# Kernel optimization log

Measured on AMD Instinct MI355X. Metric: run time of the kernel, lower is better.

## Reference

```python
import jax, jax.numpy as jnp
import numpy as np

# Dims
B_, L_, IN_ = 16, 8192, 57
DM, DS, HD, EXP, NL, OUT = 64, 32, 32, 2, 2, 6
DI = EXP * DM            # 128 inner dim
NH = DI // HD            # 4 heads
DPROJ = 2 * DI + 2 * DS + NH  # z, x, B, C, dt


def setup_inputs() -> dict:
    key = jax.random.key(0)
    ks = jax.random.split(key, 8)
    def rn(k, shape, scale=0.02):
        return jax.random.normal(k, shape, dtype=jnp.float32) * scale
    return {
        "x": jax.random.normal(ks[0], (B_, L_, IN_), dtype=jnp.float32),
        "W_in": rn(ks[1], (IN_, DM)),
        "b_in": jnp.zeros((DM,), jnp.float32),
        "in_proj_W": rn(ks[2], (NL, DM, DPROJ)),
        "in_proj_b": jnp.zeros((NL, DPROJ), jnp.float32),
        "A_log": jnp.log(jnp.broadcast_to(jnp.arange(1, NH + 1, dtype=jnp.float32), (NL, NH))),
        "D": jnp.ones((NL, NH), jnp.float32),
        "dt_bias": rn(ks[3], (NL, NH), 0.1),
        "out_proj_W": rn(ks[4], (NL, DI, DM)),
        "out_proj_b": jnp.zeros((NL, DM), jnp.float32),
        "cls_W": rn(ks[5], (DM, OUT)),
        "cls_b": jnp.zeros((OUT,), jnp.float32),
    }


def _mamba_layer(x, W, b, A_log, D, dt_bias, Wo, bo):
    """SISO Mamba3-style selective scan block. x: [B, L, DM]."""
    Bsz, L, _ = x.shape
    zxbcdt = x @ W + b                               # [B, L, DPROJ]
    z, xin, Bm, Cm, dt = jnp.split(
        zxbcdt, [DI, 2 * DI, 2 * DI + DS, 2 * DI + 2 * DS], axis=-1)
    dt = jax.nn.softplus(dt + dt_bias)               # [B, L, NH]
    A = -jnp.exp(A_log)                              # [NH], per-head scalar (SISO)
    xin = jax.nn.silu(xin).reshape(Bsz, L, NH, HD)   # [B, L, NH, HD]
    Bm = jax.nn.silu(Bm)                             # [B, L, DS]
    Cm = jax.nn.silu(Cm)                             # [B, L, DS]
    decay = jnp.exp(dt * A)                          # [B, L, NH]

    def step(h, inp):
        # h: [B, NH, HD, DS]
        xt, bt, ct, dtt, dect = inp
        h = dect[:, :, None, None] * h + (dtt[:, :, None] * xt)[..., None] * bt[:, None, None, :]
        yt = jnp.einsum('bhpn,bn->bhp', h, ct)       # [B, NH, HD]
        return h, yt

    h0 = jnp.zeros((Bsz, NH, HD, DS), x.dtype)
    xs = (jnp.moveaxis(xin, 1, 0), jnp.moveaxis(Bm, 1, 0), jnp.moveaxis(Cm, 1, 0),
          jnp.moveaxis(dt, 1, 0), jnp.moveaxis(decay, 1, 0))
    _, ys = jax.lax.scan(step, h0, xs)               # [L, B, NH, HD]
    y = jnp.moveaxis(ys, 0, 1) + D[None, None, :, None] * xin
    y = y.reshape(Bsz, L, DI) * jax.nn.silu(z)       # gated output
    return y @ Wo + bo                               # [B, L, DM]


def reference(x, W_in, b_in, in_proj_W, in_proj_b, A_log, D, dt_bias,
              out_proj_W, out_proj_b, cls_W, cls_b):
    h = x @ W_in + b_in                              # linear_in
    for l in range(NL):                              # residual Mamba stack
        h = h + _mamba_layer(h, in_proj_W[l], in_proj_b[l], A_log[l], D[l],
                             dt_bias[l], out_proj_W[l], out_proj_b[l])
    pooled = h.mean(axis=1)                          # AdaptiveAvgPool1d(1)
    return pooled @ cls_W + cls_b                    # classifier [B, OUT]
```

## Files before the change

kernel.cpp:

```cpp
#include <hip/hip_runtime.h>

#define BSZ   16
#define LSEQ  8192
#define DMDL  64
#define DSD   32
#define HDD   32
#define NHD   4
#define DIN   128
#define NLAY  2
#define NOUTC 6
#define DPRJ  324
#define QC    64
#define NCH   128
#define NT21  21

typedef __attribute__((ext_vector_type(8))) short bf16x8;
typedef __attribute__((ext_vector_type(4))) float f32x4;

__device__ float          g_h0[BSZ*LSEQ*DMDL];
__device__ unsigned short g_xy[BSZ*LSEQ*DIN];
__device__ unsigned short g_Ca[BSZ*LSEQ*DSD];
__device__ float          g_pc[BSZ*LSEQ*NHD];
__device__ unsigned short g_cS[BSZ*NCH*NHD*HDD*DSD];
__device__ unsigned short g_Hb[BSZ*NCH*NHD*HDD*DSD];
__device__ float          g_cL[BSZ*NCH*NHD];
__device__ float          g_ppc[BSZ*NCH*DMDL];
__device__ unsigned short g_wf[NLAY*NT21*2*64*8];
__device__ unsigned short g_wo[NLAY*4*4*64*8];

__device__ __forceinline__ float silu_f(float v){ return v / (1.0f + __expf(-v)); }
__device__ __forceinline__ float softplus_f(float v){ return (v > 15.0f) ? v : __logf(1.0f + __expf(v)); }
__device__ __forceinline__ unsigned short f2bf(float f){
  union { float f; unsigned u; } v; v.f = f;
  unsigned r = v.u + 0x7FFFu + ((v.u >> 16) & 1u);
  return (unsigned short)(r >> 16);
}
__device__ __forceinline__ float bf2f(unsigned short h){
  union { unsigned u; float f; } v; v.u = ((unsigned)h) << 16;
  return v.f;
}
__device__ __forceinline__ unsigned cvtpk(float lo, float hi){
  unsigned r;
  asm("v_cvt_pk_bf16_f32 %0, %1, %2" : "=v"(r) : "v"(lo), "v"(hi));
  return r;
}

#define LSTR 132
__global__ __launch_bounds__(256) void k_linin(
    const float* __restrict__ x, const float* __restrict__ W,
    const float* __restrict__ bias)
{
  __shared__ float xt[57*LSTR];
  __shared__ float wl[57*64];
  const int tid = threadIdx.x;
  const long tb = (long)blockIdx.x * 128;
  for (int i = tid; i < 912; i += 256)
    *(float4*)&wl[i*4] = *(const float4*)&W[i*4];
  for (int i = tid; i < 1824; i += 256){
    float4 v = *(const float4*)&x[tb*57 + (long)i*4];
    const int e = i*4;
    int t0 = e / 57;
    int k0 = e - t0*57;
    float vv[4] = {v.x, v.y, v.z, v.w};
    #pragma unroll
    for (int j = 0; j < 4; ++j){
      int t = t0, k = k0 + j;
      if (k >= 57){ t += 1; k -= 57; }
      xt[k*LSTR + t] = vv[j];
    }
  }
  __syncthreads();
  const int d0 = (tid & 7) * 8;
  const int t0 = (tid >> 3) * 4;
  float acc[4][8];
  #pragma unroll
  for (int i = 0; i < 4; ++i)
    #pragma unroll
    for (int j = 0; j < 8; ++j) acc[i][j] = 0.f;
  #pragma unroll 4
  for (int k = 0; k < 57; ++k){
    float4 xv4 = *(const float4*)&xt[k*LSTR + t0];
    float4 w0  = *(const float4*)&wl[k*64 + d0];
    float4 w1  = *(const float4*)&wl[k*64 + d0 + 4];
    float xv[4] = {xv4.x, xv4.y, xv4.z, xv4.w};
    float wv[8] = {w0.x, w0.y, w0.z, w0.w, w1.x, w1.y, w1.z, w1.w};
    #pragma unroll
    for (int i = 0; i < 4; ++i)
      #pragma unroll
      for (int j = 0; j < 8; ++j) acc[i][j] += xv[i] * wv[j];
  }
  float4 bb0 = *(const float4*)&bias[d0];
  float4 bb1 = *(const float4*)&bias[d0 + 4];
  #pragma unroll
  for (int i = 0; i < 4; ++i){
    float4 o0, o1;
    o0.x = acc[i][0] + bb0.x; o0.y = acc[i][1] + bb0.y;
    o0.z = acc[i][2] + bb0.z; o0.w = acc[i][3] + bb0.w;
    o1.x = acc[i][4] + bb1.x; o1.y = acc[i][5] + bb1.y;
    o1.z = acc[i][6] + bb1.z; o1.w = acc[i][7] + bb1.w;
    *(float4*)&g_h0[(tb + t0 + i)*64 + d0]     = o0;
    *(float4*)&g_h0[(tb + t0 + i)*64 + d0 + 4] = o1;
  }
}

__global__ __launch_bounds__(128) void k_wprep(const float* __restrict__ W)
{
  const int nt = blockIdx.x;
  const int l  = blockIdx.y;
  const int ks = threadIdx.x >> 6, lane = threadIdx.x & 63;
  const float* Wl = W + (long)l*64*DPRJ;
  const int n  = nt*16 + (lane & 15);
  const int k0 = ks*32 + (lane >> 4)*8;
  unsigned short v[8];
  #pragma unroll
  for (int j = 0; j < 8; ++j)
    v[j] = (n < DPRJ) ? f2bf(Wl[(k0 + j)*DPRJ + n]) : (unsigned short)0;
  unsigned short* d = &g_wf[((((long)l*NT21 + nt)*2 + ks)*64 + lane)*8];
  *(ushort4*)&d[0] = make_ushort4(v[0], v[1], v[2], v[3]);
  *(ushort4*)&d[4] = make_ushort4(v[4], v[5], v[6], v[7]);
}

__global__ __launch_bounds__(64) void k_wprep2(const float* __restrict__ Wo)
{
  const int nt = blockIdx.x >> 2, ks = blockIdx.x & 3, l = blockIdx.y;
  const int lane = threadIdx.x;
  const int n  = nt*16 + (lane & 15);
  const int k0 = ks*32 + (lane >> 4)*8;
  const float* Wl = Wo + (long)l*128*64;
  unsigned short* d = &g_wo[((((long)l*4 + nt)*4 + ks)*64 + lane)*8];
  unsigned short v[8];
  #pragma unroll
  for (int j = 0; j < 8; ++j) v[j] = f2bf(Wl[(k0 + j)*64 + n]);
  *(ushort4*)&d[0] = make_ushort4(v[0], v[1], v[2], v[3]);
  *(ushort4*)&d[4] = make_ushort4(v[4], v[5], v[6], v[7]);
}

#define SB 40
#define ST 72
__device__ __forceinline__ int xsw(int p, int s){
  return p*ST + (((((s) >> 3) + ((p) >> 2)) & 7) << 3) + ((s) & 7);
}
__device__ __forceinline__ int xsw8(int p, int blk){
  return p*ST + (((((blk)) + ((p) >> 2)) & 7) << 3);
}
__global__ __launch_bounds__(256) void k_ps(
    const float* __restrict__ ipb, const float* __restrict__ dtb,
    const float* __restrict__ A_log, const float* __restrict__ Dp, int l)
{
  __shared__ __align__(16) unsigned short AfrX[4096];
  __shared__ __align__(16) unsigned short Bb[64*SB];
  __shared__ __align__(16) unsigned short Cb[64*SB];
  __shared__ __align__(16) unsigned short Bbt[32*ST];
  __shared__ __align__(16) unsigned short Xt0[32*ST];
  __shared__ __align__(16) unsigned short Mb[2*64*ST];
  __shared__ float Sl[4*64];
  __shared__ float dts[4*64];
  __shared__ float wls[4*64];
  __shared__ float dtl[64*4];
  const int tid = threadIdx.x;
  const int cI = blockIdx.x, b = blockIdx.y;
  const long tb = (long)b*LSEQ + (long)cI*QC;
  for (int i = tid; i < 512; i += 256){
    const int t = i >> 3, k8 = i & 7;
    float4 f0 = *(const float4*)&g_h0[(tb + t)*64 + k8*8];
    float4 f1 = *(const float4*)&g_h0[(tb + t)*64 + k8*8 + 4];
    const int mt = t >> 4, ks = k8 >> 2, q = k8 & 3, ln = (t & 15) + 16*q;
    uint4 pk;
    pk.x = cvtpk(f0.x, f0.y); pk.y = cvtpk(f0.z, f0.w);
    pk.z = cvtpk(f1.x, f1.y); pk.w = cvtpk(f1.z, f1.w);
    *(uint4*)&AfrX[(((mt*2 + ks)*64) + ln)*8] = pk;
  }
  __syncthreads();
  const int w = tid >> 6, lane = tid & 63;
  const int colq = lane & 15, rowq = lane >> 4;
  const int t4 = w*16 + rowq*4;
  const float* bl = ipb + (long)l*DPRJ;
  const unsigned short* wf = &g_wf[(long)l*NT21*2*64*8];
  const bf16x8 a0 = *(const bf16x8*)&AfrX[((w*2 + 0)*64 + lane)*8];
  const bf16x8 a1 = *(const bf16x8*)&AfrX[((w*2 + 1)*64 + lane)*8];
  #pragma unroll
  for (int nti = 0; nti < 4; ++nti){
    const int nt = 16 + nti;
    bf16x8 b0 = *(const bf16x8*)&wf[((nt*2 + 0)*64 + lane)*8];
    bf16x8 b1 = *(const bf16x8*)&wf[((nt*2 + 1)*64 + lane)*8];
    const float bia = bl[nt*16 + colq];
    f32x4 acc = {0.f, 0.f, 0.f, 0.f};
    acc = __builtin_amdgcn_mfma_f32_16x16x32_bf16(a0, b0, acc, 0, 0, 0);
    acc = __builtin_amdgcn_mfma_f32_16x16x32_bf16(a1, b1, acc, 0, 0, 0);
    const unsigned u0 = cvtpk(silu_f(acc[0] + bia), silu_f(acc[1] + bia));
    const unsigned u1 = cvtpk(silu_f(acc[2] + bia), silu_f(acc[3] + bia));
    if (nti < 2){
      const int n = nti*16 + colq;
      uint2 uu; uu.x = u0; uu.y = u1;
      *(uint2*)&Bbt[xsw(n, t4)] = uu;
      Bb[(t4 + 0)*SB + n] = (unsigned short)(u0 & 0xFFFFu);
      Bb[(t4 + 1)*SB + n] = (unsigned short)(u0 >> 16);
      Bb[(t4 + 2)*SB + n] = (unsigned short)(u1 & 0xFFFFu);
      Bb[(t4 + 3)*SB + n] = (unsigned short)(u1 >> 16);
    } else {
      const int n = (nti - 2)*16 + colq;
      Cb[(t4 + 0)*SB + n] = (unsigned short)(u0 & 0xFFFFu);
      Cb[(t4 + 1)*SB + n] = (unsigned short)(u0 >> 16);
      Cb[(t4 + 2)*SB + n] = (unsigned short)(u1 & 0xFFFFu);
      Cb[(t4 + 3)*SB + n] = (unsigned short)(u1 >> 16);
    }
  }
  {
    bf16x8 b0 = *(const bf16x8*)&wf[((20*2 + 0)*64 + lane)*8];
    bf16x8 b1 = *(const bf16x8*)&wf[((20*2 + 1)*64 + lane)*8];
    f32x4 acc = {0.f, 0.f, 0.f, 0.f};
    acc = __builtin_amdgcn_mfma_f32_16x16x32_bf16(a0, b0, acc, 0, 0, 0);
    acc = __builtin_amdgcn_mfma_f32_16x16x32_bf16(a1, b1, acc, 0, 0, 0);
    if (colq < 4){
      const float bia = bl[320 + colq] + dtb[l*4 + colq];
      #pragma unroll
      for (int r = 0; r < 4; ++r)
        dtl[(t4 + r)*4 + colq] = softplus_f(acc[r] + bia);
    }
  }
  __syncthreads();
  {
    const int h = w, t = lane;
    const float Ah = -__expf(A_log[l*4 + h]);
    const float v = dtl[t*4 + h];
    float x = v * Ah;
    #pragma unroll
    for (int d = 1; d < 64; d <<= 1){
      float y = __shfl_up(x, d);
      if (t >= d) x += y;
    }
    Sl[h*64 + t] = x;
    dts[h*64 + t] = v;
    const float send = __shfl(x, 63);
    wls[h*64 + t] = __expf(send - x) * v;
    if (t == 63) g_cL[((long)b*NCH + cI)*4 + h] = x;
    g_pc[(tb + t)*4 + h] = __expf(x);
  }
  {
    const int t = tid >> 2, c0 = (tid & 3) * 8;
    *(uint4*)&g_Ca[(tb + t)*32 + c0] = *(const uint4*)&Cb[t*SB + c0];
  }
  float Greg[3][4];
  int Gmt[3], Gst[3];
  #pragma unroll
  for (int rep = 0; rep < 3; ++rep){
    const int k = w + rep*4;
    if (k < 10){
      const int mt = (k >= 6) ? 3 : ((k >= 3) ? 2 : ((k >= 1) ? 1 : 0));
      const int st = k - mt*(mt+1)/2;
      Gmt[rep] = mt; Gst[rep] = st;
      bf16x8 af = *(const bf16x8*)&Cb[(mt*16 + colq)*SB + rowq*8];
      bf16x8 bf = *(const bf16x8*)&Bb[(st*16 + colq)*SB + rowq*8];
      f32x4 acc = {0.f, 0.f, 0.f, 0.f};
      acc = __builtin_amdgcn_mfma_f32_16x16x32_bf16(af, bf, acc, 0, 0, 0);
      #pragma unroll
      for (int r = 0; r < 4; ++r) Greg[rep][r] = acc[r];
    } else { Gmt[rep] = -1; Gst[rep] = 0; }
  }
  #pragma unroll
  for (int rep = 0; rep < 2; ++rep){
    const int k = w + rep*4;
    if (k < 6){
      const int mt = (k < 3) ? 0 : ((k < 5) ? 1 : 2);
      const int st = (k < 3) ? (k + 1) : ((k < 5) ? (k - 1) : 3);
      #pragma unroll
      for (int r = 0; r < 4; ++r){
        const int t = mt*16 + rowq*4 + r, s = st*16 + colq;
        Mb[xsw(t, s)] = 0;
        Mb[64*ST + xsw(t, s)] = 0;
      }
    }
  }
  __syncthreads();
  for (int h = 0; h < NHD; ++h){
    unsigned short* Xt  = (h & 1) ? AfrX : Xt0;
    unsigned short* Mbh = Mb + (h & 1)*64*ST;
    #pragma unroll
    for (int half = 0; half < 2; ++half){
      const int nt = 8 + 2*h + half;
      bf16x8 b0 = *(const bf16x8*)&wf[((nt*2 + 0)*64 + lane)*8];
      bf16x8 b1 = *(const bf16x8*)&wf[((nt*2 + 1)*64 + lane)*8];
      const float bia = bl[nt*16 + colq];
      f32x4 acc = {0.f, 0.f, 0.f, 0.f};
      acc = __builtin_amdgcn_mfma_f32_16x16x32_bf16(a0, b0, acc, 0, 0, 0);
      acc = __builtin_amdgcn_mfma_f32_16x16x32_bf16(a1, b1, acc, 0, 0, 0);
      uint2 uu;
      uu.x = cvtpk(silu_f(acc[0] + bia), silu_f(acc[1] + bia));
      uu.y = cvtpk(silu_f(acc[2] + bia), silu_f(acc[3] + bia));
      *(uint2*)&Xt[xsw(half*16 + colq, t4)] = uu;
    }
    #pragma unroll
    for (int rep = 0; rep < 3; ++rep){
      if (Gmt[rep] >= 0){
        const int mt = Gmt[rep], st = Gst[rep];
        const int s = st*16 + colq;
        const float sls = Sl[h*64 + s];
        const float dv = dts[h*64 + s];
        #pragma unroll
        for (int r = 0; r < 4; ++r){
          const int t = mt*16 + rowq*4 + r;
          const float m = (s <= t) ? __expf(Sl[h*64 + t] - sls) * dv * Greg[rep][r] : 0.f;
          Mbh[xsw(t, s)] = f2bf(m);
        }
      }
    }
    __syncthreads();
    const float Dh = Dp[l*4 + h];
    bf16x8 ma0 = *(const bf16x8*)&Mbh[xsw8(w*16 + colq, rowq)];
    bf16x8 ma1 = *(const bf16x8*)&Mbh[xsw8(w*16 + colq, rowq + 4)];
    bf16x8 xb0, xb1;
    #pragma unroll
    for (int nt = 0; nt < 2; ++nt){
      bf16x8 b0 = *(const bf16x8*)&Xt[xsw8(nt*16 + colq, rowq)];
      bf16x8 b1 = *(const bf16x8*)&Xt[xsw8(nt*16 + colq, rowq + 4)];
      if (nt == (w & 1)){ xb0 = b0; xb1 = b1; }
      f32x4 acc = {0.f, 0.f, 0.f, 0.f};
      acc = __builtin_amdgcn_mfma_f32_16x16x32_bf16(ma0, b0, acc, 0, 0, 0);
      acc = __builtin_amdgcn_mfma_f32_16x16x32_bf16(ma1, b1, acc, 0, 0, 0);
      const int p = nt*16 + colq;
      #pragma unroll
      for (int r = 0; r < 4; ++r){
        const int t = w*16 + rowq*4 + r;
        const float xv = bf2f(Xt[xsw(p, t)]);
        g_xy[(tb + t)*128 + h*32 + p] = f2bf(acc[r] + Dh*xv);
      }
    }
    {
      union { bf16x8 v; unsigned short us[8]; } sx0, sx1;
      union { bf16x8 v; unsigned u[4]; } sa0, sa1;
      sx0.v = xb0; sx1.v = xb1;
      #pragma unroll
      for (int jj = 0; jj < 4; ++jj){
        sa0.u[jj] = cvtpk(bf2f(sx0.us[2*jj])   * wls[h*64 + rowq*8 + 2*jj],
                          bf2f(sx0.us[2*jj+1]) * wls[h*64 + rowq*8 + 2*jj + 1]);
        sa1.u[jj] = cvtpk(bf2f(sx1.us[2*jj])   * wls[h*64 + 32 + rowq*8 + 2*jj],
                          bf2f(sx1.us[2*jj+1]) * wls[h*64 + 32 + rowq*8 + 2*jj + 1]);
      }
      const int mt = w & 1, nt2 = w >> 1;
      bf16x8 bb0 = *(const bf16x8*)&Bbt[xsw8(nt2*16 + colq, rowq)];
      bf16x8 bb1 = *(const bf16x8*)&Bbt[xsw8(nt2*16 + colq, rowq + 4)];
      f32x4 acc = {0.f, 0.f, 0.f, 0.f};
      acc = __builtin_amdgcn_mfma_f32_16x16x32_bf16(sa0.v, bb0, acc, 0, 0, 0);
      acc = __builtin_amdgcn_mfma_f32_16x16x32_bf16(sa1.v, bb1, acc, 0, 0, 0);
      const long base = (((long)b*NCH + cI)*NHD + h)*(HDD*DSD);
      const int n = nt2*16 + colq;
      #pragma unroll
      for (int r = 0; r < 4; ++r){
        const int p = mt*16 + rowq*4 + r;
        g_cS[base + p*32 + n] = f2bf(acc[r]);
      }
    }
  }
}

__global__ __launch_bounds__(128) void k_s2()
{
  const int h = blockIdx.x >> 3, seg = blockIdx.x & 7, b = blockIdx.y;
  const int idx = seg*128 + threadIdx.x;
  float H = 0.f;
  #pragma unroll 4
  for (int c = 0; c < NCH; ++c){
    const long o = (((long)b*NCH + c)*NHD + h)*1024 + idx;
    const float cs = bf2f(g_cS[o]);
    const float lg = g_cL[((long)b*NCH + c)*4 + h];
    g_Hb[o] = f2bf(H);
    H = __expf(lg) * H + cs;
  }
}

__global__ __launch_bounds__(256) void k_s3(
    const float* __restrict__ ipb, const float* __restrict__ bo, int l, int finalLayer)
{
  __shared__ __align__(16) unsigned short Hb[128*40];
  __shared__ __align__(16) unsigned short Cb[64*40];
  __shared__ __align__(16) unsigned short gl[64*136];
  __shared__ float pcl[4*64];
  __shared__ float csum[4*64];
  const int tid = threadIdx.x;
  const int cI = blockIdx.x, b = blockIdx.y;
  const long tb = (long)b*LSEQ + (long)cI*QC;
  const long hbase = (((long)b*NCH + cI)*NHD)*(long)(HDD*DSD);
  for (int i = tid; i < 512; i += 256){
    const int hp = i >> 2, n0 = (i & 3) * 8;
    *(uint4*)&Hb[hp*40 + n0] = *(const uint4*)&g_Hb[hbase + hp*32 + n0];
  }
  for (int i = tid; i < 512; i += 256){
    const int t = i >> 3, n0 = (i & 7) * 4;
    *(ushort4*)&Cb[t*40 + n0] = *(const ushort4*)&g_Ca[(tb + t)*32 + n0];
  }
  { int t = tid >> 2, h = tid & 3; pcl[h*64 + t] = g_pc[(tb + t)*4 + h]; }
  __syncthreads();
  const int w = tid >> 6, lane = tid & 63;
  const int colq = lane & 15, rowq = lane >> 4;
  const float* blz = ipb + (long)l*DPRJ;
  const unsigned short* wfz = &g_wf[(long)l*NT21*2*64*8];
  {
    const long tok0 = tb + w*16 + colq;
    bf16x8 h0a, h0b;
    {
      float4 f0 = *(const float4*)&g_h0[tok0*64 + rowq*8];
      float4 f1 = *(const float4*)&g_h0[tok0*64 + rowq*8 + 4];
      float4 f2 = *(const float4*)&g_h0[tok0*64 + 32 + rowq*8];
      float4 f3 = *(const float4*)&g_h0[tok0*64 + 32 + rowq*8 + 4];
      union { bf16x8 v; unsigned u[4]; } ca, cb2;
      ca.u[0] = cvtpk(f0.x, f0.y); ca.u[1] = cvtpk(f0.z, f0.w);
      ca.u[2] = cvtpk(f1.x, f1.y); ca.u[3] = cvtpk(f1.z, f1.w);
      cb2.u[0] = cvtpk(f2.x, f2.y); cb2.u[1] = cvtpk(f2.z, f2.w);
      cb2.u[2] = cvtpk(f3.x, f3.y); cb2.u[3] = cvtpk(f3.z, f3.w);
      h0a = ca.v; h0b = cb2.v;
    }
    bf16x8 a = *(const bf16x8*)&Cb[(w*16 + colq)*40 + rowq*8];
    #pragma unroll
    for (int nt = 0; nt < 8; ++nt){
      bf16x8 bfr = *(const bf16x8*)&Hb[(nt*16 + colq)*40 + rowq*8];
      f32x4 acc = {0.f, 0.f, 0.f, 0.f};
      acc = __builtin_amdgcn_mfma_f32_16x16x32_bf16(a, bfr, acc, 0, 0, 0);
      bf16x8 bz0 = *(const bf16x8*)&wfz[((nt*2 + 0)*64 + lane)*8];
      bf16x8 bz1 = *(const bf16x8*)&wfz[((nt*2 + 1)*64 + lane)*8];
      f32x4 zac = {0.f, 0.f, 0.f, 0.f};
      zac = __builtin_amdgcn_mfma_f32_16x16x32_bf16(h0a, bz0, zac, 0, 0, 0);
      zac = __builtin_amdgcn_mfma_f32_16x16x32_bf16(h0b, bz1, zac, 0, 0, 0);
      const int hp = nt*16 + colq;
      const int h = hp >> 5;
      const float zb = blz[hp];
      #pragma unroll
      for (int r = 0; r < 4; ++r){
        const int t = w*16 + rowq*4 + r;
        const long tok = tb + t;
        const float v = pcl[h*64 + t] * acc[r] + bf2f(g_xy[tok*128 + hp]);
        gl[t*136 + hp] = f2bf(v * silu_f(zac[r] + zb));
      }
    }
  }
  __syncthreads();
  const unsigned short* wo = &g_wo[(long)l*4*4*512];
  #pragma unroll
  for (int nt2 = 0; nt2 < 4; ++nt2){
    f32x4 acc = {0.f, 0.f, 0.f, 0.f};
    #pragma unroll
    for (int ks = 0; ks < 4; ++ks){
      bf16x8 a = *(const bf16x8*)&gl[(w*16 + colq)*136 + ks*32 + rowq*8];
      bf16x8 bfr = *(const bf16x8*)&wo[(nt2*4 + ks)*512 + lane*8];
      acc = __builtin_amdgcn_mfma_f32_16x16x32_bf16(a, bfr, acc, 0, 0, 0);
    }
    const int dm = nt2*16 + colq;
    const float bb = bo[l*64 + dm];
    float part = 0.f;
    #pragma unroll
    for (int r = 0; r < 4; ++r){
      const int t = w*16 + rowq*4 + r;
      const long tok = tb + t;
      const float o = acc[r] + bb + g_h0[tok*64 + dm];
      g_h0[tok*64 + dm] = o;
      part += o;
    }
    if (finalLayer){
      part += __shfl_xor(part, 16);
      part += __shfl_xor(part, 32);
      if (rowq == 0) csum[w*64 + dm] = part;
    }
  }
  if (finalLayer){
    __syncthreads();
    if (tid < 64){
      g_ppc[((long)b*NCH + cI)*64 + tid] =
        csum[tid] + csum[64 + tid] + csum[128 + tid] + csum[192 + tid];
    }
  }
}

__global__ __launch_bounds__(64) void k_pool2(
    const float* __restrict__ cW, const float* __restrict__ cb,
    float* __restrict__ out)
{
  __shared__ float pl[64];
  const int b = blockIdx.x, tid = threadIdx.x;
  float s = 0.f;
  for (int c = 0; c < NCH; ++c) s += g_ppc[((long)b*NCH + c)*64 + tid];
  pl[tid] = s * (1.0f / 8192.0f);
  __syncthreads();
  if (tid < NOUTC){
    float acc = cb[tid];
    for (int dm = 0; dm < 64; ++dm) acc += pl[dm] * cW[dm*NOUTC + tid];
    out[b*NOUTC + tid] = acc;
  }
}

extern "C" void kernel_launch(void* const* d_in, const int* in_sizes, int n_in,
                              void* d_out, int out_size, void* d_ws, size_t ws_size,
                              hipStream_t stream)
{
  const float* x      = (const float*)d_in[0];
  const float* W_in   = (const float*)d_in[1];
  const float* b_in   = (const float*)d_in[2];
  const float* ipW    = (const float*)d_in[3];
  const float* ipb    = (const float*)d_in[4];
  const float* A_log  = (const float*)d_in[5];
  const float* Dp     = (const float*)d_in[6];
  const float* dtb    = (const float*)d_in[7];
  const float* opW    = (const float*)d_in[8];
  const float* opb    = (const float*)d_in[9];
  const float* clsW   = (const float*)d_in[10];
  const float* clsb   = (const float*)d_in[11];
  float* out = (float*)d_out;
  (void)d_ws; (void)ws_size;

  k_wprep<<<dim3(NT21, NLAY), 128, 0, stream>>>(ipW);
  k_wprep2<<<dim3(16, NLAY), 64, 0, stream>>>(opW);
  k_linin<<<1024, 256, 0, stream>>>(x, W_in, b_in);
  for (int l = 0; l < NLAY; ++l){
    k_ps<<<dim3(NCH, BSZ), 256, 0, stream>>>(ipb, dtb, A_log, Dp, l);
    k_s2<<<dim3(32, BSZ), 128, 0, stream>>>();
    k_s3<<<dim3(NCH, BSZ), 256, 0, stream>>>(ipb, opb, l, (l == NLAY-1) ? 1 : 0);
  }
  k_pool2<<<BSZ, 64, 0, stream>>>(clsW, clsb, out);
}
```

Baseline: 310.8 us.

## Store intra-chunk y in MFMA fragment layout and prefetch next head weights

The intra-chunk output y (g_xy) is now written in the MFMA accumulator fragment order, as one packed 8-byte store per lane instead of scattered 2-byte stores. k_s3 reads it back with a matching ushort4 load, replacing strided per-element global gathers. k_ps also prefetches the next head's x-projection weights and biases into registers while the current head is processed. It reuses the B/C staging buffer as the second M buffer to cut shared memory use. The aliasing depends on Bb and Cb being dead by head 1, and the extra live registers may raise pressure.

```diff
diff --git a/kernel.cpp b/kernel.cpp
--- a/kernel.cpp
+++ b/kernel.cpp
@@ -148,11 +148,10 @@
     const float* __restrict__ A_log, const float* __restrict__ Dp, int l)
 {
   __shared__ __align__(16) unsigned short AfrX[4096];
-  __shared__ __align__(16) unsigned short Bb[64*SB];
-  __shared__ __align__(16) unsigned short Cb[64*SB];
+  __shared__ __align__(16) unsigned short U[2*64*SB];
   __shared__ __align__(16) unsigned short Bbt[32*ST];
   __shared__ __align__(16) unsigned short Xt0[32*ST];
-  __shared__ __align__(16) unsigned short Mb[2*64*ST];
+  __shared__ __align__(16) unsigned short Mb0[64*ST];
   __shared__ float Sl[4*64];
   __shared__ float dts[4*64];
   __shared__ float wls[4*64];
@@ -160,6 +159,10 @@
   const int tid = threadIdx.x;
   const int cI = blockIdx.x, b = blockIdx.y;
   const long tb = (long)b*LSEQ + (long)cI*QC;
+  const long bc = (long)b*NCH + cI;
+  unsigned short* Bb = U;
+  unsigned short* Cb = U + 64*SB;
+  unsigned short* Mb1 = U;
   for (int i = tid; i < 512; i += 256){
     const int t = i >> 3, k8 = i & 7;
     float4 f0 = *(const float4*)&g_h0[(tb + t)*64 + k8*8];
@@ -233,7 +236,7 @@
     dts[h*64 + t] = v;
     const float send = __shfl(x, 63);
     wls[h*64 + t] = __expf(send - x) * v;
-    if (t == 63) g_cL[((long)b*NCH + cI)*4 + h] = x;
+    if (t == 63) g_cL[(bc)*4 + h] = x;
     g_pc[(tb + t)*4 + h] = __expf(x);
   }
   {
@@ -266,28 +269,61 @@
       #pragma unroll
       for (int r = 0; r < 4; ++r){
         const int t = mt*16 + rowq*4 + r, s = st*16 + colq;
-        Mb[xsw(t, s)] = 0;
-        Mb[64*ST + xsw(t, s)] = 0;
-      }
-    }
-  }
+        Mb0[xsw(t, s)] = 0;
+      }
+    }
+  }
+  bf16x8 cw0, cw1, cw2, cw3;
+  float cbia0, cbia1;
+  cw0 = *(const bf16x8*)&wf[((8*2 + 0)*64 + lane)*8];
+  cw1 = *(const bf16x8*)&wf[((8*2 + 1)*64 + lane)*8];
+  cw2 = *(const bf16x8*)&wf[((9*2 + 0)*64 + lane)*8];
+  cw3 = *(const bf16x8*)&wf[((9*2 + 1)*64 + lane)*8];
+  cbia0 = bl[8*16 + colq];
+  cbia1 = bl[9*16 + colq];
   __syncthreads();
   for (int h = 0; h < NHD; ++h){
     unsigned short* Xt  = (h & 1) ? AfrX : Xt0;
-    unsigned short* Mbh = Mb + (h & 1)*64*ST;
-    #pragma unroll
-    for (int half = 0; half < 2; ++half){
-      const int nt = 8 + 2*h + half;
-      bf16x8 b0 = *(const bf16x8*)&wf[((nt*2 + 0)*64 + lane)*8];
-      bf16x8 b1 = *(const bf16x8*)&wf[((nt*2 + 1)*64 + lane)*8];
-      const float bia = bl[nt*16 + colq];
+    unsigned short* Mbh = (h & 1) ? Mb1 : Mb0;
+    {
       f32x4 acc = {0.f, 0.f, 0.f, 0.f};
-      acc = __builtin_amdgcn_mfma_f32_16x16x32_bf16(a0, b0, acc, 0, 0, 0);
-      acc = __builtin_amdgcn_mfma_f32_16x16x32_bf16(a1, b1, acc, 0, 0, 0);
+      acc = __builtin_amdgcn_mfma_f32_16x16x32_bf16(a0, cw0, acc, 0, 0, 0);
+      acc = __builtin_amdgcn_mfma_f32_16x16x32_bf16(a1, cw1, acc, 0, 0, 0);
       uint2 uu;
-      uu.x = cvtpk(silu_f(acc[0] + bia), silu_f(acc[1] + bia));
-      uu.y = cvtpk(silu_f(acc[2] + bia), silu_f(acc[3] + bia));
-      *(uint2*)&Xt[xsw(half*16 + colq, t4)] = uu;
+      uu.x = cvtpk(silu_f(acc[0] + cbia0), silu_f(acc[1] + cbia0));
+      uu.y = cvtpk(silu_f(acc[2] + cbia0), silu_f(acc[3] + cbia0));
+      *(uint2*)&Xt[xsw(colq, t4)] = uu;
+    }
+    {
+      f32x4 acc = {0.f, 0.f, 0.f, 0.f};
+      acc = __builtin_amdgcn_mfma_f32_16x16x32_bf16(a0, cw2, acc, 0, 0, 0);
+      acc = __builtin_amdgcn_mfma_f32_16x16x32_bf16(a1, cw3, acc, 0, 0, 0);
+      uint2 uu;
+      uu.x = cvtpk(silu_f(acc[0] + cbia1), silu_f(acc[1] + cbia1));
+      uu.y = cvtpk(silu_f(acc[2] + cbia1), silu_f(acc[3] + cbia1));
+      *(uint2*)&Xt[xsw(16 + colq, t4)] = uu;
+    }
+    const int hn = (h + 1) & 3;
+    bf16x8 nw0 = *(const bf16x8*)&wf[(((8 + 2*hn)*2 + 0)*64 + lane)*8];
+    bf16x8 nw1 = *(const bf16x8*)&wf[(((8 + 2*hn)*2 + 1)*64 + lane)*8];
+    bf16x8 nw2 = *(const bf16x8*)&wf[(((9 + 2*hn)*2 + 0)*64 + lane)*8];
+    bf16x8 nw3 = *(const bf16x8*)&wf[(((9 + 2*hn)*2 + 1)*64 + lane)*8];
+    const float nbia0 = bl[(8 + 2*hn)*16 + colq];
+    const float nbia1 = bl[(9 + 2*hn)*16 + colq];
+    if (h == 1){
+      #pragma unroll
+      for (int rep = 0; rep < 2; ++rep){
+        const int k = w + rep*4;
+        if (k < 6){
+          const int mt = (k < 3) ? 0 : ((k < 5) ? 1 : 2);
+          const int st = (k < 3) ? (k + 1) : ((k < 5) ? (k - 1) : 3);
+          #pragma unroll
+          for (int r = 0; r < 4; ++r){
+            const int t = mt*16 + rowq*4 + r, s = st*16 + colq;
+            Mb1[xsw(t, s)] = 0;
+          }
+        }
+      }
     }
     #pragma unroll
     for (int rep = 0; rep < 3; ++rep){
@@ -318,12 +354,17 @@
       acc = __builtin_amdgcn_mfma_f32_16x16x32_bf16(ma0, b0, acc, 0, 0, 0);
       acc = __builtin_amdgcn_mfma_f32_16x16x32_bf16(ma1, b1, acc, 0, 0, 0);
       const int p = nt*16 + colq;
+      float yv[4];
       #pragma unroll
       for (int r = 0; r < 4; ++r){
         const int t = w*16 + rowq*4 + r;
-        const float xv = bf2f(Xt[xsw(p, t)]);
-        g_xy[(tb + t)*128 + h*32 + p] = f2bf(acc[r] + Dh*xv);
-      }
+        yv[r] = acc[r] + Dh * bf2f(Xt[xsw(p, t)]);
+      }
+      uint2 uu;
+      uu.x = cvtpk(yv[0], yv[1]);
+      uu.y = cvtpk(yv[2], yv[3]);
+      const long ybase = ((((bc*NHD + h)*4 + w)*2 + nt)*256);
+      *(uint2*)&g_xy[ybase + lane*4] = uu;
     }
     {
       union { bf16x8 v; unsigned short us[8]; } sx0, sx1;
@@ -342,7 +383,7 @@
       f32x4 acc = {0.f, 0.f, 0.f, 0.f};
       acc = __builtin_amdgcn_mfma_f32_16x16x32_bf16(sa0.v, bb0, acc, 0, 0, 0);
       acc = __builtin_amdgcn_mfma_f32_16x16x32_bf16(sa1.v, bb1, acc, 0, 0, 0);
-      const long base = (((long)b*NCH + cI)*NHD + h)*(HDD*DSD);
+      const long base = ((bc*NHD + h))*(long)(HDD*DSD);
       const int n = nt2*16 + colq;
       #pragma unroll
       for (int r = 0; r < 4; ++r){
@@ -350,6 +391,8 @@
         g_cS[base + p*32 + n] = f2bf(acc[r]);
       }
     }
+    cw0 = nw0; cw1 = nw1; cw2 = nw2; cw3 = nw3;
+    cbia0 = nbia0; cbia1 = nbia1;
   }
 }
 
@@ -379,7 +422,8 @@
   const int tid = threadIdx.x;
   const int cI = blockIdx.x, b = blockIdx.y;
   const long tb = (long)b*LSEQ + (long)cI*QC;
-  const long hbase = (((long)b*NCH + cI)*NHD)*(long)(HDD*DSD);
+  const long bc = (long)b*NCH + cI;
+  const long hbase = (bc*NHD)*(long)(HDD*DSD);
   for (int i = tid; i < 512; i += 256){
     const int hp = i >> 2, n0 = (i & 3) * 8;
     *(uint4*)&Hb[hp*40 + n0] = *(const uint4*)&g_Hb[hbase + hp*32 + n0];
@@ -421,13 +465,14 @@
       zac = __builtin_amdgcn_mfma_f32_16x16x32_bf16(h0a, bz0, zac, 0, 0, 0);
       zac = __builtin_amdgcn_mfma_f32_16x16x32_bf16(h0b, bz1, zac, 0, 0, 0);
       const int hp = nt*16 + colq;
-      const int h = hp >> 5;
+      const int h = nt >> 1, ntp = nt & 1;
       const float zb = blz[hp];
+      const ushort4 yv = *(const ushort4*)&g_xy[(((bc*NHD + h)*4 + w)*2 + ntp)*256 + lane*4];
+      const float yf[4] = {bf2f(yv.x), bf2f(yv.y), bf2f(yv.z), bf2f(yv.w)};
       #pragma unroll
       for (int r = 0; r < 4; ++r){
         const int t = w*16 + rowq*4 + r;
-        const long tok = tb + t;
-        const float v = pcl[h*64 + t] * acc[r] + bf2f(g_xy[tok*128 + hp]);
+        const float v = pcl[h*64 + t] * acc[r] + yf[r];
         gl[t*136 + hp] = f2bf(v * silu_f(zac[r] + zb));
       }
     }
```

Result: faster. 300.8 us (-3.2%).
